# Optimization experiments

Hardware: AMD Instinct MI355X
Metric: run time of the kernel (lower is better)

## Reference

```python
import jax, jax.numpy as jnp
import numpy as np

B = 262144      # batch of states (PPO rollout)
J = 16          # num_pools -> state_dim=32, action_dim=256
M = 12          # num_epochs_per_day (experts)
H = 34          # hidden_dim (fixed in source)
A = J * J


def setup_inputs() -> dict:
    key = jax.random.key(0)
    ks = jax.random.split(key, 6)
    states = jax.random.normal(ks[0], (B, 2 * J), dtype=jnp.float32)
    epoch_idx = jax.random.randint(ks[1], (B,), 0, M, dtype=jnp.int32)
    # fc1: kaiming normal (relu), zero bias
    W1 = jax.random.normal(ks[2], (H, 2 * J), dtype=jnp.float32) * np.sqrt(2.0 / (2 * J))
    b1 = jnp.zeros((H,), dtype=jnp.float32)
    # m expert output layers [M, A, H]
    Wout = jax.random.normal(ks[3], (M, A, H), dtype=jnp.float32) * np.sqrt(1.0 / H)
    bout = jax.random.normal(ks[4], (M, A), dtype=jnp.float32) * np.sqrt(1.0 / H)
    mask = jax.random.randint(ks[5], (J, J), 0, 2, dtype=jnp.int32)
    return {"states": states, "epoch_idx": epoch_idx, "W1": W1, "b1": b1,
            "Wout": Wout, "bout": bout, "mask": mask}


def reference(states, epoch_idx, W1, b1, Wout, bout, mask):
    # shared trunk: [B, H]
    x = jax.nn.relu(jnp.einsum('bs,hs->bh', states, W1) + b1)
    # grouped expert GEMM via one-hot routing (equivalent to output_layers[epoch_idx])
    onehot = jax.nn.one_hot(epoch_idx, M, dtype=x.dtype)           # [B, M]
    xe = x[:, None, :] * onehot[:, :, None]                        # [B, M, H]
    logits = jnp.einsum('bmh,mah->ba', xe, Wout) + bout[epoch_idx]  # [B, A]
    logits = logits.reshape(-1, J, J)
    NEG = jnp.float32(-1e9)
    return jnp.where(mask == 0, NEG, logits)
```

## Files before the change

kernel.cpp:

```cpp
#include <hip/hip_runtime.h>

typedef __attribute__((ext_vector_type(8))) short short8;
typedef __attribute__((ext_vector_type(4))) float f32x4;
typedef __attribute__((ext_vector_type(4))) int   i32x4;

#define SDIM 32
#define HDIM 34
#define NEXP 12
#define ACOL 256
#define SPB  256
#define MAXROWS 448
#define STG_STRIDE 260

#define BAR_LGKM() asm volatile("s_waitcnt lgkmcnt(0)\n\ts_barrier" ::: "memory")

__device__ __forceinline__ unsigned int bpack(float lo, float hi) {
    unsigned int a = __builtin_bit_cast(unsigned int, lo);
    unsigned int b = __builtin_bit_cast(unsigned int, hi);
    return ((a + 0x8000u) >> 16) | ((b + 0x8000u) & 0xffff0000u);
}

__global__ __launch_bounds__(256) void k0_wpack(
    const float* __restrict__ Wout, uint4* __restrict__ wpack,
    unsigned int* __restrict__ w2p)
{
    const int tid = blockIdx.x * 256 + threadIdx.x;
    if (tid >= NEXP * 4 * 4 * 64) return;
    const int lane = tid & 63;
    const int j    = (tid >> 6) & 3;
    const int wvv  = (tid >> 8) & 3;
    const int e    = tid >> 10;
    const int r = lane & 15, g = lane >> 4;
    const int col = wvv * 64 + j * 16 + r;
    const float* wr = Wout + ((size_t)e * ACOL + col) * HDIM;
    uint4 q;
    q.x = bpack(wr[g*8+0], wr[g*8+1]);
    q.y = bpack(wr[g*8+2], wr[g*8+3]);
    q.z = bpack(wr[g*8+4], wr[g*8+5]);
    q.w = bpack(wr[g*8+6], wr[g*8+7]);
    wpack[tid] = q;
    if (tid < NEXP * ACOL) {
        const float* wr2 = Wout + (size_t)tid * HDIM;
        w2p[tid] = bpack(wr2[32], wr2[33]);
    }
}

__global__ __launch_bounds__(256, 2) void actor_kernel(
    const float* __restrict__ states,
    const int*   __restrict__ epoch_idx,
    const float* __restrict__ W1,
    const float* __restrict__ b1,
    const uint4* __restrict__ wpack,
    const unsigned int* __restrict__ w2p,
    const float* __restrict__ bout,
    const int*   __restrict__ mask,
    float*       __restrict__ out,
    int nB)
{
    __shared__ __align__(16) unsigned int xs[MAXROWS * 16];
    __shared__ unsigned int   xt[MAXROWS];
    __shared__ unsigned short rowid[MAXROWS];
    __shared__ __align__(16) float stg[2][16 * STG_STRIDE];
    __shared__ int cnt[NEXP], goff[NEXP], ntl[NEXP];

    float* w1s = &stg[0][0];
    float* b1s = w1s + HDIM * SDIM;

    const int t  = threadIdx.x;
    const int s0 = blockIdx.x * SPB;

    for (int i = t; i < HDIM * SDIM; i += 256) w1s[i] = W1[i];
    if (t < HDIM) b1s[t] = b1[t];
    if (t < NEXP) cnt[t] = 0;
    for (int i = t; i < MAXROWS; i += 256) rowid[i] = 0xFFFFu;

    const int  sidx  = s0 + t;
    const bool valid = (sidx < nB);
    float sr[SDIM];
    int e = 0;
    if (valid) {
        const f32x4* sp = (const f32x4*)(states + (size_t)sidx * SDIM);
        #pragma unroll
        for (int q = 0; q < SDIM / 4; ++q) {
            f32x4 v = sp[q];
            sr[4*q+0] = v[0]; sr[4*q+1] = v[1]; sr[4*q+2] = v[2]; sr[4*q+3] = v[3];
        }
        e = epoch_idx[sidx];
    }
    __syncthreads();

    int rank = 0;
    if (valid) rank = atomicAdd(&cnt[e], 1);
    __syncthreads();

    if (t == 0) {
        int base = 0;
        #pragma unroll
        for (int i = 0; i < NEXP; ++i) {
            goff[i] = base;
            int nt = (cnt[i] + 15) >> 4;
            ntl[i] = nt;
            base += nt << 4;
        }
    }
    float x[HDIM];
    if (valid) {
        #pragma unroll 2
        for (int h = 0; h < HDIM; ++h) {
            float acc = b1s[h];
            const float4* wr = (const float4*)(w1s + h * SDIM);
            #pragma unroll
            for (int q = 0; q < SDIM / 4; ++q) {
                float4 wv = wr[q];
                acc = fmaf(sr[4*q+0], wv.x, acc);
                acc = fmaf(sr[4*q+1], wv.y, acc);
                acc = fmaf(sr[4*q+2], wv.z, acc);
                acc = fmaf(sr[4*q+3], wv.w, acc);
            }
            x[h] = fmaxf(acc, 0.0f);
        }
    }
    __syncthreads();

    if (valid) {
        const int slot = goff[e] + rank;
        const unsigned sw = (((unsigned)slot >> 2) & 3u) << 4;
        char* rbase = (char*)xs + slot * 64;
        unsigned d[16];
        #pragma unroll
        for (int k = 0; k < 16; ++k) d[k] = bpack(x[2*k], x[2*k+1]);
        #pragma unroll
        for (int c = 0; c < 4; ++c) {
            f32x4 q;
            q[0] = __builtin_bit_cast(float, d[4*c+0]);
            q[1] = __builtin_bit_cast(float, d[4*c+1]);
            q[2] = __builtin_bit_cast(float, d[4*c+2]);
            q[3] = __builtin_bit_cast(float, d[4*c+3]);
            *(f32x4*)(rbase + (((unsigned)(c * 16)) ^ sw)) = q;
        }
        xt[slot]    = bpack(x[32], x[33]);
        rowid[slot] = (unsigned short)t;
    }
    __syncthreads();

    const int wv   = t >> 6;
    const int lane = t & 63;
    const int r    = lane & 15;
    const int g    = lane >> 4;
    const int colbase = wv * 64 + r;
    const float NEG = -1e9f;
    const i32x4 mq = *(const i32x4*)(mask + 4 * lane);

    float* outb = out + (size_t)s0 * ACOL;
    int buf = 0;

    for (int e2 = 0; e2 < NEXP; ++e2) {
        const int ntiles = ntl[e2];
        if (ntiles == 0) continue;

        short8   bf1[4];
        unsigned w2[4];
        float    bias[4];
        const uint4* wp = wpack + ((size_t)(e2 * 4 + wv) * 4) * 64 + lane;
        #pragma unroll
        for (int j = 0; j < 4; ++j) {
            bf1[j]  = __builtin_bit_cast(short8, wp[j * 64]);
            w2[j]   = (g == 0) ? w2p[e2 * ACOL + colbase + j * 16] : 0u;
            bias[j] = bout[e2 * ACOL + colbase + j * 16];
        }

        const int tb = goff[e2];
        for (int st = 0; st < ntiles; ++st) {
            const int rb  = tb + (st << 4);
            const int row = rb + r;
            const unsigned sw = (((unsigned)row >> 2) & 3u) << 4;
            const char* rp = (const char*)xs + row * 64;
            short8 a1 = *(const short8*)(rp + (((unsigned)(g * 16)) ^ sw));
            short8 a2 = __builtin_bit_cast(short8,
                          make_uint4(g == 0 ? xt[row] : 0u, 0u, 0u, 0u));

            #pragma unroll
            for (int j = 0; j < 4; ++j) {
                f32x4 a = {bias[j], bias[j], bias[j], bias[j]};
                a = __builtin_amdgcn_mfma_f32_16x16x32_bf16(a1, bf1[j], a, 0, 0, 0);
                short8 b2 = __builtin_bit_cast(short8,
                              make_uint4(w2[j], 0u, 0u, 0u));
                a = __builtin_amdgcn_mfma_f32_16x16x32_bf16(a2, b2, a, 0, 0, 0);
                const int c = colbase + 16 * j;
                #pragma unroll
                for (int i = 0; i < 4; ++i)
                    stg[buf][(g * 4 + i) * STG_STRIDE + c] = a[i];
            }

            BAR_LGKM();

            f32x4 v[4];
            unsigned rid[4];
            #pragma unroll
            for (int q = 0; q < 4; ++q) {
                const int lrow = wv * 4 + q;
                rid[q] = rowid[rb + lrow];
                v[q]   = *(const f32x4*)&stg[buf][lrow * STG_STRIDE + 4 * lane];
            }
            #pragma unroll
            for (int q = 0; q < 4; ++q) {
                f32x4 w = v[q];
                w[0] = mq[0] ? w[0] : NEG;
                w[1] = mq[1] ? w[1] : NEG;
                w[2] = mq[2] ? w[2] : NEG;
                w[3] = mq[3] ? w[3] : NEG;
                if (rid[q] != 0xFFFFu)
                    *(f32x4*)(outb + (size_t)rid[q] * ACOL + 4 * lane) = w;
            }
            buf ^= 1;
        }
    }
}

extern "C" void kernel_launch(void* const* d_in, const int* in_sizes, int n_in,
                              void* d_out, int out_size, void* d_ws, size_t ws_size,
                              hipStream_t stream) {
    const float* states    = (const float*)d_in[0];
    const int*   epoch_idx = (const int*)  d_in[1];
    const float* W1        = (const float*)d_in[2];
    const float* b1        = (const float*)d_in[3];
    const float* Wout      = (const float*)d_in[4];
    const float* bout      = (const float*)d_in[5];
    const int*   mask      = (const int*)  d_in[6];
    float*       out       = (float*)d_out;

    const int nB   = in_sizes[0] / SDIM;
    const int grid = (nB + SPB - 1) / SPB;

    uint4*        wpack = (uint4*)d_ws;
    unsigned int* w2p   = (unsigned int*)((char*)d_ws + 196608);

    k0_wpack<<<48, 256, 0, stream>>>(Wout, wpack, w2p);
    actor_kernel<<<grid, 256, 0, stream>>>(states, epoch_idx, W1, b1,
                                           wpack, w2p, bout, mask, out, nB);
}
```

Baseline: 87.38 us.

## Split fused actor kernel into separate trunk and grouped-GEMM kernels via global workspace

Splits the single fused kernel into two. A trunk kernel computes the hidden activations and buckets the rows by expert, writing them to global workspace. A GEMM kernel then reads them back and runs the expert MFMAs. The GEMM kernel stages each wave's results in its own LDS slab, so it needs no block barrier. Stores become scalar per-lane writes of only the valid rows instead of the old vector stores. The intent is smaller per-kernel LDS and higher occupancy (launch bounds 4), at the cost of an extra launch and a global round-trip of the bucketed activations, plus narrower output stores.

```diff
diff --git a/kernel.cpp b/kernel.cpp
--- a/kernel.cpp
+++ b/kernel.cpp
@@ -2,17 +2,13 @@
 
 typedef __attribute__((ext_vector_type(8))) short short8;
 typedef __attribute__((ext_vector_type(4))) float f32x4;
-typedef __attribute__((ext_vector_type(4))) int   i32x4;
 
 #define SDIM 32
 #define HDIM 34
 #define NEXP 12
 #define ACOL 256
 #define SPB  256
-#define MAXROWS 448
-#define STG_STRIDE 260
-
-#define BAR_LGKM() asm volatile("s_waitcnt lgkmcnt(0)\n\ts_barrier" ::: "memory")
+#define ROWS 448
 
 __device__ __forceinline__ unsigned int bpack(float lo, float hi) {
     unsigned int a = __builtin_bit_cast(unsigned int, lo);
@@ -45,36 +41,23 @@
     }
 }
 
-__global__ __launch_bounds__(256, 2) void actor_kernel(
-    const float* __restrict__ states,
-    const int*   __restrict__ epoch_idx,
-    const float* __restrict__ W1,
-    const float* __restrict__ b1,
-    const uint4* __restrict__ wpack,
-    const unsigned int* __restrict__ w2p,
-    const float* __restrict__ bout,
-    const int*   __restrict__ mask,
-    float*       __restrict__ out,
-    int nB)
+__global__ __launch_bounds__(256, 4) void k3_trunk(
+    const float* __restrict__ states, const int* __restrict__ epoch_idx,
+    const float* __restrict__ W1, const float* __restrict__ b1,
+    uint4* __restrict__ xg, unsigned int* __restrict__ xtg,
+    unsigned short* __restrict__ ridg, int* __restrict__ meta, int nB)
 {
-    __shared__ __align__(16) unsigned int xs[MAXROWS * 16];
-    __shared__ unsigned int   xt[MAXROWS];
-    __shared__ unsigned short rowid[MAXROWS];
-    __shared__ __align__(16) float stg[2][16 * STG_STRIDE];
-    __shared__ int cnt[NEXP], goff[NEXP], ntl[NEXP];
-
-    float* w1s = &stg[0][0];
-    float* b1s = w1s + HDIM * SDIM;
-
-    const int t  = threadIdx.x;
-    const int s0 = blockIdx.x * SPB;
-
+    __shared__ float w1s[HDIM * SDIM];
+    __shared__ float b1s[HDIM];
+    __shared__ int cnt[NEXP], goff[NEXP];
+
+    const int t = threadIdx.x;
+    const int b = blockIdx.x;
     for (int i = t; i < HDIM * SDIM; i += 256) w1s[i] = W1[i];
     if (t < HDIM) b1s[t] = b1[t];
     if (t < NEXP) cnt[t] = 0;
-    for (int i = t; i < MAXROWS; i += 256) rowid[i] = 0xFFFFu;
-
-    const int  sidx  = s0 + t;
+
+    const int  sidx  = b * SPB + t;
     const bool valid = (sidx < nB);
     float sr[SDIM];
     int e = 0;
@@ -98,9 +81,7 @@
         #pragma unroll
         for (int i = 0; i < NEXP; ++i) {
             goff[i] = base;
-            int nt = (cnt[i] + 15) >> 4;
-            ntl[i] = nt;
-            base += nt << 4;
+            base += ((cnt[i] + 15) >> 4) << 4;
         }
     }
     float x[HDIM];
@@ -124,39 +105,62 @@
 
     if (valid) {
         const int slot = goff[e] + rank;
-        const unsigned sw = (((unsigned)slot >> 2) & 3u) << 4;
-        char* rbase = (char*)xs + slot * 64;
-        unsigned d[16];
-        #pragma unroll
-        for (int k = 0; k < 16; ++k) d[k] = bpack(x[2*k], x[2*k+1]);
-        #pragma unroll
-        for (int c = 0; c < 4; ++c) {
-            f32x4 q;
-            q[0] = __builtin_bit_cast(float, d[4*c+0]);
-            q[1] = __builtin_bit_cast(float, d[4*c+1]);
-            q[2] = __builtin_bit_cast(float, d[4*c+2]);
-            q[3] = __builtin_bit_cast(float, d[4*c+3]);
-            *(f32x4*)(rbase + (((unsigned)(c * 16)) ^ sw)) = q;
-        }
-        xt[slot]    = bpack(x[32], x[33]);
-        rowid[slot] = (unsigned short)t;
-    }
-    __syncthreads();
-
-    const int wv   = t >> 6;
-    const int lane = t & 63;
-    const int r    = lane & 15;
-    const int g    = lane >> 4;
-    const int colbase = wv * 64 + r;
+        unsigned d[17];
+        #pragma unroll
+        for (int k = 0; k < 17; ++k) d[k] = bpack(x[2*k], x[2*k+1]);
+        uint4* xr = xg + ((size_t)b * ROWS + slot) * 4;
+        xr[0] = make_uint4(d[0],  d[1],  d[2],  d[3]);
+        xr[1] = make_uint4(d[4],  d[5],  d[6],  d[7]);
+        xr[2] = make_uint4(d[8],  d[9],  d[10], d[11]);
+        xr[3] = make_uint4(d[12], d[13], d[14], d[15]);
+        xtg[b * ROWS + slot]  = d[16];
+        ridg[b * ROWS + slot] = (unsigned short)t;
+    }
+    if (t < NEXP) {
+        meta[b * 24 + t]        = goff[t];
+        meta[b * 24 + NEXP + t] = cnt[t];
+    }
+}
+
+__global__ __launch_bounds__(256, 4) void k4_gemm(
+    const uint4* __restrict__ wpack, const unsigned int* __restrict__ w2p,
+    const float* __restrict__ bout, const int* __restrict__ mask,
+    const uint4* __restrict__ xg, const unsigned int* __restrict__ xtg,
+    const unsigned short* __restrict__ ridg, const int* __restrict__ meta,
+    float* __restrict__ out)
+{
+    __shared__ float slab[4][16 * 68];
+    __shared__ unsigned short lrid[ROWS];
+    __shared__ int lgoff[NEXP], lcnt[NEXP];
+
+    const int t = threadIdx.x;
+    const int b = blockIdx.x;
+
+    if (t < NEXP) {
+        lgoff[t] = meta[b * 24 + t];
+        lcnt[t]  = meta[b * 24 + NEXP + t];
+    }
+    {
+        const uint* rsrc = (const uint*)(ridg + b * ROWS);
+        uint* rdst = (uint*)lrid;
+        if (t < ROWS / 2) rdst[t] = rsrc[t];
+    }
+    __syncthreads();
+
+    const int wv = t >> 6, lane = t & 63;
+    const int r = lane & 15, g = lane >> 4;
+    const int m = mask[wv * 64 + lane];
     const float NEG = -1e9f;
-    const i32x4 mq = *(const i32x4*)(mask + 4 * lane);
-
-    float* outb = out + (size_t)s0 * ACOL;
-    int buf = 0;
+    const int s0 = b * SPB;
+    float* mystg = slab[wv];
+    const uint4*        xb  = xg  + ((size_t)b * ROWS) * 4;
+    const unsigned int* xtb = xtg + b * ROWS;
 
     for (int e2 = 0; e2 < NEXP; ++e2) {
-        const int ntiles = ntl[e2];
-        if (ntiles == 0) continue;
+        const int nv = lcnt[e2];
+        if (nv == 0) continue;
+        const int ntiles = (nv + 15) >> 4;
+        const int tb = lgoff[e2];
 
         short8   bf1[4];
         unsigned w2[4];
@@ -165,54 +169,38 @@
         #pragma unroll
         for (int j = 0; j < 4; ++j) {
             bf1[j]  = __builtin_bit_cast(short8, wp[j * 64]);
-            w2[j]   = (g == 0) ? w2p[e2 * ACOL + colbase + j * 16] : 0u;
-            bias[j] = bout[e2 * ACOL + colbase + j * 16];
-        }
-
-        const int tb = goff[e2];
+            w2[j]   = (g == 0) ? w2p[e2 * ACOL + wv * 64 + j * 16 + r] : 0u;
+            bias[j] = bout[e2 * ACOL + wv * 64 + j * 16 + r];
+        }
+
         for (int st = 0; st < ntiles; ++st) {
             const int rb  = tb + (st << 4);
             const int row = rb + r;
-            const unsigned sw = (((unsigned)row >> 2) & 3u) << 4;
-            const char* rp = (const char*)xs + row * 64;
-            short8 a1 = *(const short8*)(rp + (((unsigned)(g * 16)) ^ sw));
+            short8 a1 = __builtin_bit_cast(short8, xb[row * 4 + g]);
             short8 a2 = __builtin_bit_cast(short8,
-                          make_uint4(g == 0 ? xt[row] : 0u, 0u, 0u, 0u));
+                          make_uint4(g == 0 ? xtb[row] : 0u, 0u, 0u, 0u));
 
             #pragma unroll
             for (int j = 0; j < 4; ++j) {
                 f32x4 a = {bias[j], bias[j], bias[j], bias[j]};
                 a = __builtin_amdgcn_mfma_f32_16x16x32_bf16(a1, bf1[j], a, 0, 0, 0);
-                short8 b2 = __builtin_bit_cast(short8,
-                              make_uint4(w2[j], 0u, 0u, 0u));
+                short8 b2 = __builtin_bit_cast(short8, make_uint4(w2[j], 0u, 0u, 0u));
                 a = __builtin_amdgcn_mfma_f32_16x16x32_bf16(a2, b2, a, 0, 0, 0);
-                const int c = colbase + 16 * j;
                 #pragma unroll
                 for (int i = 0; i < 4; ++i)
-                    stg[buf][(g * 4 + i) * STG_STRIDE + c] = a[i];
+                    mystg[(4 * g + i) * 68 + 16 * j + r] = a[i];
             }
 
-            BAR_LGKM();
-
-            f32x4 v[4];
-            unsigned rid[4];
+            const int nrow = nv - (st << 4);
             #pragma unroll
-            for (int q = 0; q < 4; ++q) {
-                const int lrow = wv * 4 + q;
-                rid[q] = rowid[rb + lrow];
-                v[q]   = *(const f32x4*)&stg[buf][lrow * STG_STRIDE + 4 * lane];
+            for (int lrow = 0; lrow < 16; ++lrow) {
+                if (lrow < nrow) {
+                    const int rid = lrid[rb + lrow];
+                    float v = mystg[lrow * 68 + lane];
+                    v = m ? v : NEG;
+                    out[(size_t)(s0 + rid) * ACOL + wv * 64 + lane] = v;
+                }
             }
-            #pragma unroll
-            for (int q = 0; q < 4; ++q) {
-                f32x4 w = v[q];
-                w[0] = mq[0] ? w[0] : NEG;
-                w[1] = mq[1] ? w[1] : NEG;
-                w[2] = mq[2] ? w[2] : NEG;
-                w[3] = mq[3] ? w[3] : NEG;
-                if (rid[q] != 0xFFFFu)
-                    *(f32x4*)(outb + (size_t)rid[q] * ACOL + 4 * lane) = w;
-            }
-            buf ^= 1;
         }
     }
 }
@@ -230,12 +218,23 @@
     float*       out       = (float*)d_out;
 
     const int nB   = in_sizes[0] / SDIM;
-    const int grid = (nB + SPB - 1) / SPB;
-
-    uint4*        wpack = (uint4*)d_ws;
-    unsigned int* w2p   = (unsigned int*)((char*)d_ws + 196608);
+    const int nblk = (nB + SPB - 1) / SPB;
+
+    char* ws = (char*)d_ws;
+    size_t o = 0;
+    uint4*          wpack = (uint4*)(ws + o);        o += 196608;
+    unsigned int*   w2p   = (unsigned int*)(ws + o); o += 12288;
+    int*            meta  = (int*)(ws + o);          o += (size_t)nblk * 24 * 4;
+    o = (o + 255) & ~(size_t)255;
+    unsigned short* ridg  = (unsigned short*)(ws + o); o += (size_t)nblk * ROWS * 2;
+    o = (o + 255) & ~(size_t)255;
+    unsigned int*   xtg   = (unsigned int*)(ws + o); o += (size_t)nblk * ROWS * 4;
+    o = (o + 255) & ~(size_t)255;
+    uint4*          xg    = (uint4*)(ws + o);
 
     k0_wpack<<<48, 256, 0, stream>>>(Wout, wpack, w2p);
-    actor_kernel<<<grid, 256, 0, stream>>>(states, epoch_idx, W1, b1,
-                                           wpack, w2p, bout, mask, out, nB);
-}
+    k3_trunk<<<nblk, 256, 0, stream>>>(states, epoch_idx, W1, b1,
+                                       xg, xtg, ridg, meta, nB);
+    k4_gemm<<<nblk, 256, 0, stream>>>(wpack, w2p, bout, mask,
+                                      xg, xtg, ridg, meta, out);
+}
```

New measurement: 127.1 us. 45.4% more time.

## Replace per-expert row sorting with per-tile expert bitmask and masked MFMA accumulation

Applied to the files above, without the earlier changes.

Rows are no longer bucketed by expert through atomics and prefix offsets. Each 16-row tile now records a bitmask of the experts present, and for each such expert it runs MFMAs with the A operand zeroed for rows that belong to other experts, prefetching the next expert's weights while the current one computes. The bias is folded into the MFMA through an extra packed bf16 column, and each wave stages its results in a private slab, so the block-wide barriers inside the tile loop go away. Occupancy is raised to 4 blocks per CU. The cost is redundant MFMA work when tiles mix many experts (likely with random routing over 12 experts), and the bias is now rounded to bf16.

```diff
diff --git a/kernel.cpp b/kernel.cpp
--- a/kernel.cpp
+++ b/kernel.cpp
@@ -2,17 +2,14 @@
 
 typedef __attribute__((ext_vector_type(8))) short short8;
 typedef __attribute__((ext_vector_type(4))) float f32x4;
-typedef __attribute__((ext_vector_type(4))) int   i32x4;
 
 #define SDIM 32
 #define HDIM 34
 #define NEXP 12
 #define ACOL 256
 #define SPB  256
-#define MAXROWS 448
-#define STG_STRIDE 260
-
-#define BAR_LGKM() asm volatile("s_waitcnt lgkmcnt(0)\n\ts_barrier" ::: "memory")
+#define NT   (SPB / 16)
+#define SLAB 68
 
 __device__ __forceinline__ unsigned int bpack(float lo, float hi) {
     unsigned int a = __builtin_bit_cast(unsigned int, lo);
@@ -21,49 +18,49 @@
 }
 
 __global__ __launch_bounds__(256) void k0_wpack(
-    const float* __restrict__ Wout, uint4* __restrict__ wpack,
-    unsigned int* __restrict__ w2p)
+    const float* __restrict__ Wout, const float* __restrict__ bout,
+    uint4* __restrict__ wpack, uint2* __restrict__ w2b)
 {
     const int tid = blockIdx.x * 256 + threadIdx.x;
-    if (tid >= NEXP * 4 * 4 * 64) return;
-    const int lane = tid & 63;
-    const int j    = (tid >> 6) & 3;
-    const int wvv  = (tid >> 8) & 3;
-    const int e    = tid >> 10;
-    const int r = lane & 15, g = lane >> 4;
-    const int col = wvv * 64 + j * 16 + r;
-    const float* wr = Wout + ((size_t)e * ACOL + col) * HDIM;
-    uint4 q;
-    q.x = bpack(wr[g*8+0], wr[g*8+1]);
-    q.y = bpack(wr[g*8+2], wr[g*8+3]);
-    q.z = bpack(wr[g*8+4], wr[g*8+5]);
-    q.w = bpack(wr[g*8+6], wr[g*8+7]);
-    wpack[tid] = q;
+    if (tid < NEXP * 4 * 4 * 64) {
+        const int lane = tid & 63;
+        const int j    = (tid >> 6) & 3;
+        const int wvv  = (tid >> 8) & 3;
+        const int e    = tid >> 10;
+        const int r = lane & 15, g = lane >> 4;
+        const int col = wvv * 64 + j * 16 + r;
+        const float* wr = Wout + ((size_t)e * ACOL + col) * HDIM;
+        uint4 q;
+        q.x = bpack(wr[g*8+0], wr[g*8+1]);
+        q.y = bpack(wr[g*8+2], wr[g*8+3]);
+        q.z = bpack(wr[g*8+4], wr[g*8+5]);
+        q.w = bpack(wr[g*8+6], wr[g*8+7]);
+        wpack[tid] = q;
+    }
     if (tid < NEXP * ACOL) {
         const float* wr2 = Wout + (size_t)tid * HDIM;
-        w2p[tid] = bpack(wr2[32], wr2[33]);
-    }
-}
-
-__global__ __launch_bounds__(256, 2) void actor_kernel(
+        w2b[tid] = make_uint2(bpack(wr2[32], wr2[33]), bpack(bout[tid], 0.0f));
+    }
+}
+
+__global__ __launch_bounds__(256, 4) void actor_kernel(
     const float* __restrict__ states,
     const int*   __restrict__ epoch_idx,
     const float* __restrict__ W1,
     const float* __restrict__ b1,
     const uint4* __restrict__ wpack,
-    const unsigned int* __restrict__ w2p,
-    const float* __restrict__ bout,
+    const uint2* __restrict__ w2b,
     const int*   __restrict__ mask,
     float*       __restrict__ out,
     int nB)
 {
-    __shared__ __align__(16) unsigned int xs[MAXROWS * 16];
-    __shared__ unsigned int   xt[MAXROWS];
-    __shared__ unsigned short rowid[MAXROWS];
-    __shared__ __align__(16) float stg[2][16 * STG_STRIDE];
-    __shared__ int cnt[NEXP], goff[NEXP], ntl[NEXP];
-
-    float* w1s = &stg[0][0];
+    __shared__ __align__(16) unsigned int xs[SPB * 16];
+    __shared__ uint2        xt2[SPB];
+    __shared__ int          expl[SPB];
+    __shared__ unsigned int tmask[NT];
+    __shared__ __align__(16) float slab[4][16 * SLAB];
+
+    float* w1s = &slab[0][0];
     float* b1s = w1s + HDIM * SDIM;
 
     const int t  = threadIdx.x;
@@ -71,8 +68,7 @@
 
     for (int i = t; i < HDIM * SDIM; i += 256) w1s[i] = W1[i];
     if (t < HDIM) b1s[t] = b1[t];
-    if (t < NEXP) cnt[t] = 0;
-    for (int i = t; i < MAXROWS; i += 256) rowid[i] = 0xFFFFu;
+    if (t < NT) tmask[t] = 0u;
 
     const int  sidx  = s0 + t;
     const bool valid = (sidx < nB);
@@ -89,20 +85,9 @@
     }
     __syncthreads();
 
-    int rank = 0;
-    if (valid) rank = atomicAdd(&cnt[e], 1);
-    __syncthreads();
-
-    if (t == 0) {
-        int base = 0;
-        #pragma unroll
-        for (int i = 0; i < NEXP; ++i) {
-            goff[i] = base;
-            int nt = (cnt[i] + 15) >> 4;
-            ntl[i] = nt;
-            base += nt << 4;
-        }
-    }
+    if (valid) atomicOr(&tmask[t >> 4], 1u << e);
+    expl[t] = valid ? e : 64;
+
     float x[HDIM];
     if (valid) {
         #pragma unroll 2
@@ -120,15 +105,13 @@
             x[h] = fmaxf(acc, 0.0f);
         }
     }
-    __syncthreads();
 
     if (valid) {
-        const int slot = goff[e] + rank;
-        const unsigned sw = (((unsigned)slot >> 2) & 3u) << 4;
-        char* rbase = (char*)xs + slot * 64;
-        unsigned d[16];
-        #pragma unroll
-        for (int k = 0; k < 16; ++k) d[k] = bpack(x[2*k], x[2*k+1]);
+        unsigned d[17];
+        #pragma unroll
+        for (int k = 0; k < 17; ++k) d[k] = bpack(x[2*k], x[2*k+1]);
+        const unsigned sw = ((unsigned)t >> 2) & 3u;
+        char* rbase = (char*)xs + t * 64;
         #pragma unroll
         for (int c = 0; c < 4; ++c) {
             f32x4 q;
@@ -136,10 +119,9 @@
             q[1] = __builtin_bit_cast(float, d[4*c+1]);
             q[2] = __builtin_bit_cast(float, d[4*c+2]);
             q[3] = __builtin_bit_cast(float, d[4*c+3]);
-            *(f32x4*)(rbase + (((unsigned)(c * 16)) ^ sw)) = q;
-        }
-        xt[slot]    = bpack(x[32], x[33]);
-        rowid[slot] = (unsigned short)t;
+            *(f32x4*)(rbase + ((unsigned)(c ^ sw) << 4)) = q;
+        }
+        xt2[t] = make_uint2(d[16], bpack(1.0f, 0.0f));
     }
     __syncthreads();
 
@@ -147,72 +129,74 @@
     const int lane = t & 63;
     const int r    = lane & 15;
     const int g    = lane >> 4;
-    const int colbase = wv * 64 + r;
+    const int m    = mask[wv * 64 + lane];
     const float NEG = -1e9f;
-    const i32x4 mq = *(const i32x4*)(mask + 4 * lane);
-
-    float* outb = out + (size_t)s0 * ACOL;
-    int buf = 0;
-
-    for (int e2 = 0; e2 < NEXP; ++e2) {
-        const int ntiles = ntl[e2];
-        if (ntiles == 0) continue;
-
-        short8   bf1[4];
-        unsigned w2[4];
-        float    bias[4];
-        const uint4* wp = wpack + ((size_t)(e2 * 4 + wv) * 4) * 64 + lane;
+    float* mystg = slab[wv];
+    float* outw  = out + (size_t)s0 * ACOL + wv * 64 + lane;
+    const short8 z8 = __builtin_bit_cast(short8, make_uint4(0u, 0u, 0u, 0u));
+
+    for (int tile = 0; tile < NT; ++tile) {
+        const int rb  = tile << 4;
+        const int row = rb + r;
+        const char* rp = (const char*)xs + row * 64;
+        short8 a1 = *(const short8*)(rp + ((((unsigned)g ^ (((unsigned)row >> 2) & 3u))) << 4));
+        const uint2 x2 = xt2[row];
+        const short8 at = (g == 0)
+            ? __builtin_bit_cast(short8, make_uint4(x2.x, x2.y, 0u, 0u)) : z8;
+        const int er = expl[row];
+        unsigned pm = tmask[tile];
+
+        f32x4 acc[4];
+        #pragma unroll
+        for (int j = 0; j < 4; ++j) acc[j] = f32x4{0.f, 0.f, 0.f, 0.f};
+
+        if (pm) {
+            int e2 = (int)__builtin_ctz(pm); pm &= pm - 1;
+            const uint4* wp = wpack + ((size_t)(e2 * 4 + wv) * 4) * 64 + lane;
+            uint4 fc0 = wp[0], fc1 = wp[64], fc2 = wp[128], fc3 = wp[192];
+            const uint2* tb = w2b + e2 * ACOL + wv * 64 + r;
+            uint2 tc0 = tb[0], tc1 = tb[16], tc2 = tb[32], tc3 = tb[48];
+
+            while (true) {
+                int en = -1;
+                uint4 fn0, fn1, fn2, fn3; uint2 tn0, tn1, tn2, tn3;
+                if (pm) {
+                    en = (int)__builtin_ctz(pm); pm &= pm - 1;
+                    const uint4* wpn = wpack + ((size_t)(en * 4 + wv) * 4) * 64 + lane;
+                    fn0 = wpn[0]; fn1 = wpn[64]; fn2 = wpn[128]; fn3 = wpn[192];
+                    const uint2* tbn = w2b + en * ACOL + wv * 64 + r;
+                    tn0 = tbn[0]; tn1 = tbn[16]; tn2 = tbn[32]; tn3 = tbn[48];
+                }
+                const bool mt = (er == e2);
+                const short8 a1m = mt ? a1 : z8;
+                const short8 a2m = mt ? at : z8;
+                acc[0] = __builtin_amdgcn_mfma_f32_16x16x32_bf16(a1m, __builtin_bit_cast(short8, fc0), acc[0], 0, 0, 0);
+                acc[0] = __builtin_amdgcn_mfma_f32_16x16x32_bf16(a2m, __builtin_bit_cast(short8, make_uint4(tc0.x, tc0.y, 0u, 0u)), acc[0], 0, 0, 0);
+                acc[1] = __builtin_amdgcn_mfma_f32_16x16x32_bf16(a1m, __builtin_bit_cast(short8, fc1), acc[1], 0, 0, 0);
+                acc[1] = __builtin_amdgcn_mfma_f32_16x16x32_bf16(a2m, __builtin_bit_cast(short8, make_uint4(tc1.x, tc1.y, 0u, 0u)), acc[1], 0, 0, 0);
+                acc[2] = __builtin_amdgcn_mfma_f32_16x16x32_bf16(a1m, __builtin_bit_cast(short8, fc2), acc[2], 0, 0, 0);
+                acc[2] = __builtin_amdgcn_mfma_f32_16x16x32_bf16(a2m, __builtin_bit_cast(short8, make_uint4(tc2.x, tc2.y, 0u, 0u)), acc[2], 0, 0, 0);
+                acc[3] = __builtin_amdgcn_mfma_f32_16x16x32_bf16(a1m, __builtin_bit_cast(short8, fc3), acc[3], 0, 0, 0);
+                acc[3] = __builtin_amdgcn_mfma_f32_16x16x32_bf16(a2m, __builtin_bit_cast(short8, make_uint4(tc3.x, tc3.y, 0u, 0u)), acc[3], 0, 0, 0);
+                if (en < 0) break;
+                e2 = en;
+                fc0 = fn0; fc1 = fn1; fc2 = fn2; fc3 = fn3;
+                tc0 = tn0; tc1 = tn1; tc2 = tn2; tc3 = tn3;
+            }
+        }
+
         #pragma unroll
         for (int j = 0; j < 4; ++j) {
-            bf1[j]  = __builtin_bit_cast(short8, wp[j * 64]);
-            w2[j]   = (g == 0) ? w2p[e2 * ACOL + colbase + j * 16] : 0u;
-            bias[j] = bout[e2 * ACOL + colbase + j * 16];
-        }
-
-        const int tb = goff[e2];
-        for (int st = 0; st < ntiles; ++st) {
-            const int rb  = tb + (st << 4);
-            const int row = rb + r;
-            const unsigned sw = (((unsigned)row >> 2) & 3u) << 4;
-            const char* rp = (const char*)xs + row * 64;
-            short8 a1 = *(const short8*)(rp + (((unsigned)(g * 16)) ^ sw));
-            short8 a2 = __builtin_bit_cast(short8,
-                          make_uint4(g == 0 ? xt[row] : 0u, 0u, 0u, 0u));
-
             #pragma unroll
-            for (int j = 0; j < 4; ++j) {
-                f32x4 a = {bias[j], bias[j], bias[j], bias[j]};
-                a = __builtin_amdgcn_mfma_f32_16x16x32_bf16(a1, bf1[j], a, 0, 0, 0);
-                short8 b2 = __builtin_bit_cast(short8,
-                              make_uint4(w2[j], 0u, 0u, 0u));
-                a = __builtin_amdgcn_mfma_f32_16x16x32_bf16(a2, b2, a, 0, 0, 0);
-                const int c = colbase + 16 * j;
-                #pragma unroll
-                for (int i = 0; i < 4; ++i)
-                    stg[buf][(g * 4 + i) * STG_STRIDE + c] = a[i];
-            }
-
-            BAR_LGKM();
-
-            f32x4 v[4];
-            unsigned rid[4];
-            #pragma unroll
-            for (int q = 0; q < 4; ++q) {
-                const int lrow = wv * 4 + q;
-                rid[q] = rowid[rb + lrow];
-                v[q]   = *(const f32x4*)&stg[buf][lrow * STG_STRIDE + 4 * lane];
-            }
-            #pragma unroll
-            for (int q = 0; q < 4; ++q) {
-                f32x4 w = v[q];
-                w[0] = mq[0] ? w[0] : NEG;
-                w[1] = mq[1] ? w[1] : NEG;
-                w[2] = mq[2] ? w[2] : NEG;
-                w[3] = mq[3] ? w[3] : NEG;
-                if (rid[q] != 0xFFFFu)
-                    *(f32x4*)(outb + (size_t)rid[q] * ACOL + 4 * lane) = w;
-            }
-            buf ^= 1;
+            for (int i = 0; i < 4; ++i)
+                mystg[(4 * g + i) * SLAB + 16 * j + r] = acc[j][i];
+        }
+        #pragma unroll
+        for (int lrow = 0; lrow < 16; ++lrow) {
+            float v = mystg[lrow * SLAB + lane];
+            v = m ? v : NEG;
+            if (s0 + rb + lrow < nB)
+                outw[(size_t)(rb + lrow) * ACOL] = v;
         }
     }
 }
@@ -232,10 +216,10 @@
     const int nB   = in_sizes[0] / SDIM;
     const int grid = (nB + SPB - 1) / SPB;
 
-    uint4*        wpack = (uint4*)d_ws;
-    unsigned int* w2p   = (unsigned int*)((char*)d_ws + 196608);
-
-    k0_wpack<<<48, 256, 0, stream>>>(Wout, wpack, w2p);
+    uint4* wpack = (uint4*)d_ws;
+    uint2* w2b   = (uint2*)((char*)d_ws + 196608);
+
+    k0_wpack<<<48, 256, 0, stream>>>(Wout, bout, wpack, w2b);
     actor_kernel<<<grid, 256, 0, stream>>>(states, epoch_idx, W1, b1,
-                                           wpack, w2p, bout, mask, out, nB);
-}
+                                           wpack, w2b, mask, out, nB);
+}
```

Measured after the change: 188.6 us. +115.9%, slower.

## Stage logits as single-buffered bf16 in LDS to raise occupancy

Applied to the files above, without the earlier changes.

The LDS staging buffer for MFMA results shrinks from two fp32 buffers to one bf16 buffer, and an extra barrier is added before the writes to replace the double-buffering. The bias is now added after unpacking, loaded as a vector per lane, and launch bounds are raised to 4 blocks per CU. The aim is to cut LDS and register footprint so more blocks can be resident and more memory latency hidden. In exchange the pre-bias logits are rounded to bf16, which costs output precision, and each tile pays an extra barrier.

```diff
diff --git a/kernel.cpp b/kernel.cpp
--- a/kernel.cpp
+++ b/kernel.cpp
@@ -10,7 +10,7 @@
 #define ACOL 256
 #define SPB  256
 #define MAXROWS 448
-#define STG_STRIDE 260
+#define STGS 260
 
 #define BAR_LGKM() asm volatile("s_waitcnt lgkmcnt(0)\n\ts_barrier" ::: "memory")
 
@@ -45,7 +45,7 @@
     }
 }
 
-__global__ __launch_bounds__(256, 2) void actor_kernel(
+__global__ __launch_bounds__(256, 4) void actor_kernel(
     const float* __restrict__ states,
     const int*   __restrict__ epoch_idx,
     const float* __restrict__ W1,
@@ -60,10 +60,10 @@
     __shared__ __align__(16) unsigned int xs[MAXROWS * 16];
     __shared__ unsigned int   xt[MAXROWS];
     __shared__ unsigned short rowid[MAXROWS];
-    __shared__ __align__(16) float stg[2][16 * STG_STRIDE];
+    __shared__ __align__(8) unsigned short stgb[16 * STGS];
     __shared__ int cnt[NEXP], goff[NEXP], ntl[NEXP];
 
-    float* w1s = &stg[0][0];
+    float* w1s = (float*)stgb;
     float* b1s = w1s + HDIM * SDIM;
 
     const int t  = threadIdx.x;
@@ -126,9 +126,9 @@
         const int slot = goff[e] + rank;
         const unsigned sw = (((unsigned)slot >> 2) & 3u) << 4;
         char* rbase = (char*)xs + slot * 64;
-        unsigned d[16];
-        #pragma unroll
-        for (int k = 0; k < 16; ++k) d[k] = bpack(x[2*k], x[2*k+1]);
+        unsigned d[17];
+        #pragma unroll
+        for (int k = 0; k < 17; ++k) d[k] = bpack(x[2*k], x[2*k+1]);
         #pragma unroll
         for (int c = 0; c < 4; ++c) {
             f32x4 q;
@@ -152,7 +152,6 @@
     const i32x4 mq = *(const i32x4*)(mask + 4 * lane);
 
     float* outb = out + (size_t)s0 * ACOL;
-    int buf = 0;
 
     for (int e2 = 0; e2 < NEXP; ++e2) {
         const int ntiles = ntl[e2];
@@ -160,14 +159,13 @@
 
         short8   bf1[4];
         unsigned w2[4];
-        float    bias[4];
         const uint4* wp = wpack + ((size_t)(e2 * 4 + wv) * 4) * 64 + lane;
         #pragma unroll
         for (int j = 0; j < 4; ++j) {
-            bf1[j]  = __builtin_bit_cast(short8, wp[j * 64]);
-            w2[j]   = (g == 0) ? w2p[e2 * ACOL + colbase + j * 16] : 0u;
-            bias[j] = bout[e2 * ACOL + colbase + j * 16];
-        }
+            bf1[j] = __builtin_bit_cast(short8, wp[j * 64]);
+            w2[j]  = (g == 0) ? w2p[e2 * ACOL + colbase + j * 16] : 0u;
+        }
+        const f32x4 bias4 = *(const f32x4*)(bout + e2 * ACOL + 4 * lane);
 
         const int tb = goff[e2];
         for (int st = 0; st < ntiles; ++st) {
@@ -179,40 +177,47 @@
             short8 a2 = __builtin_bit_cast(short8,
                           make_uint4(g == 0 ? xt[row] : 0u, 0u, 0u, 0u));
 
+            f32x4 acc[4];
             #pragma unroll
             for (int j = 0; j < 4; ++j) {
-                f32x4 a = {bias[j], bias[j], bias[j], bias[j]};
+                f32x4 a = {0.f, 0.f, 0.f, 0.f};
                 a = __builtin_amdgcn_mfma_f32_16x16x32_bf16(a1, bf1[j], a, 0, 0, 0);
                 short8 b2 = __builtin_bit_cast(short8,
                               make_uint4(w2[j], 0u, 0u, 0u));
                 a = __builtin_amdgcn_mfma_f32_16x16x32_bf16(a2, b2, a, 0, 0, 0);
+                acc[j] = a;
+            }
+
+            BAR_LGKM();
+
+            #pragma unroll
+            for (int j = 0; j < 4; ++j) {
                 const int c = colbase + 16 * j;
                 #pragma unroll
                 for (int i = 0; i < 4; ++i)
-                    stg[buf][(g * 4 + i) * STG_STRIDE + c] = a[i];
+                    stgb[(g * 4 + i) * STGS + c] =
+                        (unsigned short)bpack(acc[j][i], 0.0f);
             }
 
             BAR_LGKM();
 
-            f32x4 v[4];
-            unsigned rid[4];
             #pragma unroll
             for (int q = 0; q < 4; ++q) {
                 const int lrow = wv * 4 + q;
-                rid[q] = rowid[rb + lrow];
-                v[q]   = *(const f32x4*)&stg[buf][lrow * STG_STRIDE + 4 * lane];
-            }
-            #pragma unroll
-            for (int q = 0; q < 4; ++q) {
-                f32x4 w = v[q];
-                w[0] = mq[0] ? w[0] : NEG;
-                w[1] = mq[1] ? w[1] : NEG;
-                w[2] = mq[2] ? w[2] : NEG;
-                w[3] = mq[3] ? w[3] : NEG;
-                if (rid[q] != 0xFFFFu)
-                    *(f32x4*)(outb + (size_t)rid[q] * ACOL + 4 * lane) = w;
-            }
-            buf ^= 1;
+                const unsigned rid = rowid[rb + lrow];
+                const uint2 du = *(const uint2*)&stgb[lrow * STGS + 4 * lane];
+                f32x4 v;
+                v[0] = __builtin_bit_cast(float, du.x << 16)        + bias4[0];
+                v[1] = __builtin_bit_cast(float, du.x & 0xffff0000u) + bias4[1];
+                v[2] = __builtin_bit_cast(float, du.y << 16)        + bias4[2];
+                v[3] = __builtin_bit_cast(float, du.y & 0xffff0000u) + bias4[3];
+                v[0] = mq[0] ? v[0] : NEG;
+                v[1] = mq[1] ? v[1] : NEG;
+                v[2] = mq[2] ? v[2] : NEG;
+                v[3] = mq[3] ? v[3] : NEG;
+                if (rid != 0xFFFFu)
+                    *(f32x4*)(outb + (size_t)rid * ACOL + 4 * lane) = v;
+            }
         }
     }
 }
```

Result: faster. 85.60 us (-2.0%).
